# Performance work log

Measured on AMD Instinct MI355X. Metric: run time of the kernel, lower is better.

The kernel has to match this reference:

```python
import jax, jax.numpy as jnp
import numpy as np

SEQ, D, HID, C = 512, 768, 128, 5
NENT, SPAN = 128, 16


def setup_inputs() -> dict:
    key = jax.random.key(0)
    ks = jax.random.split(key, 24)
    s = 0.02

    def rn(k, shape, scale=s):
        return jax.random.normal(k, shape, dtype=jnp.float32) * scale

    inp = {
        "encoder_output": rn(ks[0], (1, SEQ, D), 1.0),
        "holder_idxs": jax.random.randint(ks[1], (NENT, SPAN), 0, SEQ, dtype=jnp.int32),
        "target_idxs": jax.random.randint(ks[2], (NENT, SPAN), 0, SEQ, dtype=jnp.int32),
        "exp_idxs": jax.random.randint(ks[3], (NENT, SPAN), 0, SEQ, dtype=jnp.int32),
    }
    names = ["Wh_f", "bh_f", "Wh_b", "bh_b", "Wt_f", "bt_f", "Wt_b", "bt_b",
             "We_f", "be_f", "We_b", "be_b"]
    for n, k in zip(names, ks[4:16]):
        shape = (4 * HID, D) if n.startswith("W") else (4 * HID,)
        inp[n] = rn(k, shape)
    inp["T_he"] = rn(ks[16], (2 * HID, 2 * HID, 2 * HID))
    inp["T_te"] = rn(ks[17], (2 * HID, 2 * HID, 2 * HID))
    inp["T_cls"] = rn(ks[18], (2 * HID, C, 2 * HID))
    return inp


def _lstm_cell_step(x, W_ih, b):
    # Single LSTM step with h0=c0=0 (the torch module feeds seq_len=1 to nn.LSTM,
    # so W_hh @ h0 vanishes; b = b_ih + b_hh). Gate order: i, f, g, o.
    g = x @ W_ih.T + b                         # [n, L, 4H]
    i, f, gg, o = jnp.split(g, 4, axis=-1)
    c = jax.nn.sigmoid(i) * jnp.tanh(gg)
    return jax.nn.sigmoid(o) * jnp.tanh(c)     # h, [n, L, H]


def _lstm_pool(enc_seq, idxs, Wf, bf, Wb, bb):
    toks = enc_seq[idxs]                       # [n, L, D] gather
    h = jnp.concatenate([_lstm_cell_step(toks, Wf, bf),
                         _lstm_cell_step(toks, Wb, bb)], axis=-1)  # [n, L, 2H]
    return h.max(axis=1)                       # max-pool over span -> [n, 2H]


def reference(encoder_output, holder_idxs, target_idxs, exp_idxs,
              Wh_f, bh_f, Wh_b, bh_b, Wt_f, bt_f, Wt_b, bt_b,
              We_f, be_f, We_b, be_b, T_he, T_te, T_cls):
    enc = encoder_output[0]                    # [SEQ, D]
    He = _lstm_pool(enc, holder_idxs, Wh_f, bh_f, Wh_b, bh_b)   # [nh, 2H]
    Te = _lstm_pool(enc, target_idxs, Wt_f, bt_f, Wt_b, bt_b)   # [nt, 2H]
    Ee = _lstm_pool(enc, exp_idxs, We_f, be_f, We_b, be_b)      # [ne, 2H]

    # hep[i,k] = He[i] @ T_he @ Ee[k];  tep[j,k] = Te[j] @ T_te @ Ee[k]
    hep = jnp.einsum('ia,abc,kc->ikb', He, T_he, Ee)            # [nh, ne, 2H]
    tep = jnp.einsum('ja,abc,kc->jkb', Te, T_te, Ee)            # [nt, ne, 2H]
    # pred[i,j,k,m] = tep[j,k] @ T_cls[:,m,:] @ hep[i,k]
    pred = jnp.einsum('jkb,bmc,ikc->ijkm', tep, T_cls, hep)     # [nh, nt, ne, C]
    return pred
```

## Files before the change

### kernel.cpp

```cpp
#include <hip/hip_runtime.h>
#include <hip/hip_bf16.h>
#include <math.h>

#define DIM   768
#define HID   128
#define H2    256
#define NENT  128
#define SPAN  16
#define NCLS  5

#define POOLB_OFF 0
#define HEPB_OFF  196608
#define TEPB_OFF  (HEPB_OFF + 8388608)
#define TCLSB_OFF (TEPB_OFF + 8388608)
#define WB_OFF    (TCLSB_OFF + 655360)
#define TOKB_OFF  21168128
#define GATES_OFF (TOKB_OFF + 9437184)
#define TMPT0_OFF 21168128
#define TMPT1_OFF (TMPT0_OFF + 16777216)
#define PREDT_OFF 21168128

typedef __attribute__((ext_vector_type(8))) short bf16x8;
typedef __attribute__((ext_vector_type(4))) float f32x4;

__device__ __forceinline__ float sigmoidf_(float x) { return 1.0f / (1.0f + __expf(-x)); }

__device__ __forceinline__ unsigned short f2bf(float x) {
    __hip_bfloat16 h = __float2bfloat16(x);
    return *reinterpret_cast<unsigned short*>(&h);
}

__global__ __launch_bounds__(256)
void prep_kernel(const float* __restrict__ Whf, const float* __restrict__ Whb,
                 const float* __restrict__ Wtf, const float* __restrict__ Wtb,
                 const float* __restrict__ Wef, const float* __restrict__ Web,
                 const float* __restrict__ Tcls, const float* __restrict__ enc,
                 const int* __restrict__ idx_h, const int* __restrict__ idx_t,
                 const int* __restrict__ idx_e,
                 unsigned short* __restrict__ WB, unsigned short* __restrict__ TB,
                 unsigned short* __restrict__ tokB)
{
    const int bb = blockIdx.x;
    const int tid = threadIdx.x;
    if (bb < 1728) {
        int gid = bb * 256 + tid;
        int t2  = gid / 73728;
        int rem = gid % 73728;
        int n   = rem / 192;
        int c4  = rem % 192;
        int gate = n >> 7, j = n & 127;
        int srow = (gate == 0) ? j : (gate == 1) ? 256 + j : 384 + j;
        const float* W = (t2 == 0) ? Whf : (t2 == 1) ? Whb : (t2 == 2) ? Wtf :
                         (t2 == 3) ? Wtb : (t2 == 4) ? Wef : Web;
        float4 v = ((const float4*)(W + srow * DIM))[c4];
        unsigned short* d = WB + ((size_t)(t2 * 384 + n)) * DIM + c4 * 4;
        d[0] = f2bf(v.x); d[1] = f2bf(v.y); d[2] = f2bf(v.z); d[3] = f2bf(v.w);
    } else if (bb < 3008) {
        int idx = (bb - 1728) * 256 + tid;
        int b = idx / (NCLS * H2);
        int r = idx % (NCLS * H2);
        int m = r >> 8, c = r & 255;
        TB[((m << 8) + c) * H2 + b] = f2bf(Tcls[idx]);
    } else {
        int gid = (bb - 3008) * 256 + tid;
        int r  = gid / 192, c4 = gid % 192;
        int type = r >> 11;
        int rem  = r & 2047;
        const int* idx = (type == 0) ? idx_h : (type == 1) ? idx_t : idx_e;
        int row = idx[rem];
        float4 v = ((const float4*)(enc + (size_t)row * DIM))[c4];
        unsigned short h4[4] = { f2bf(v.x), f2bf(v.y), f2bf(v.z), f2bf(v.w) };
        *(uint2*)(tokB + (size_t)r * DIM + c4 * 4) = *(uint2*)h4;
    }
}

__global__ __launch_bounds__(256)
void gates_mfma(const unsigned short* __restrict__ tokB,
                const unsigned short* __restrict__ WB,
                float* __restrict__ gates)
{
    __shared__ unsigned short As[2][128 * 64];
    __shared__ unsigned short Bs[2][128 * 64];
    const int lbid = ((int)blockIdx.x & 7) * 36 + ((int)blockIdx.x >> 3);
    const int type = lbid / 96;
    const int rem  = lbid % 96;
    const int mb0  = (rem / 6) * 128;
    const int nb0  = (rem % 6) * 128;
    const int tid = threadIdx.x;
    const int w = tid >> 6, l = tid & 63;
    const int lr = l & 15, lg = l >> 4;
    const unsigned short* A = tokB + (size_t)type * 2048 * DIM + (size_t)mb0 * DIM;
    const unsigned short* B = WB   + (size_t)type * 768  * DIM + (size_t)nb0 * DIM;

    const int sr0 = tid >> 3;
    const int sc  = tid & 7;

    bf16x8 ra[4], rb[4];
    #define LOADT(kt)                                                        \
        {                                                                    \
            const int koff = (kt) * 64 + sc * 8;                             \
            _Pragma("unroll")                                                \
            for (int p = 0; p < 4; ++p) {                                    \
                int rr = sr0 + p * 32;                                       \
                ra[p] = *(const bf16x8*)(A + (size_t)rr * DIM + koff);       \
                rb[p] = *(const bf16x8*)(B + (size_t)rr * DIM + koff);       \
            }                                                                \
        }
    #define WRITET(buf)                                                      \
        {                                                                    \
            _Pragma("unroll")                                                \
            for (int p = 0; p < 4; ++p) {                                    \
                int rr = sr0 + p * 32;                                       \
                int bo = (rr * 128 + sc * 16) ^ ((rr & 7) << 4);             \
                *(bf16x8*)((char*)As[buf] + bo) = ra[p];                     \
                *(bf16x8*)((char*)Bs[buf] + bo) = rb[p];                     \
            }                                                                \
        }

    f32x4 acc[4][4];
    #pragma unroll
    for (int mt = 0; mt < 4; ++mt)
        #pragma unroll
        for (int nt = 0; nt < 4; ++nt) acc[mt][nt] = (f32x4){0.f, 0.f, 0.f, 0.f};

    const int am0 = (w & 1) * 64;
    const int bn0 = (w >> 1) * 64;

    LOADT(0);
    WRITET(0);
    __syncthreads();

    int cur = 0;
    #pragma unroll 1
    for (int kt = 0; kt < 12; ++kt) {
        if (kt + 1 < 12) LOADT(kt + 1);

        #pragma unroll
        for (int ks = 0; ks < 2; ++ks) {
            bf16x8 af[4], bf[4];
            #pragma unroll
            for (int mt = 0; mt < 4; ++mt) {
                int rr = am0 + mt * 16 + lr;
                int bo = (rr * 128 + ks * 64 + lg * 16) ^ ((rr & 7) << 4);
                af[mt] = *(const bf16x8*)((const char*)As[cur] + bo);
            }
            #pragma unroll
            for (int nt = 0; nt < 4; ++nt) {
                int rr = bn0 + nt * 16 + lr;
                int bo = (rr * 128 + ks * 64 + lg * 16) ^ ((rr & 7) << 4);
                bf[nt] = *(const bf16x8*)((const char*)Bs[cur] + bo);
            }
            #pragma unroll
            for (int mt = 0; mt < 4; ++mt)
                #pragma unroll
                for (int nt = 0; nt < 4; ++nt)
                    acc[mt][nt] = __builtin_amdgcn_mfma_f32_16x16x32_bf16(af[mt], bf[nt], acc[mt][nt], 0, 0, 0);
        }

        if (kt + 1 < 12) {
            WRITET(cur ^ 1);
        }
        __syncthreads();
        cur ^= 1;
    }
    #undef LOADT
    #undef WRITET

    float* C = gates + (size_t)type * 2048 * 768 + (size_t)mb0 * 768 + nb0;
    #pragma unroll
    for (int mt = 0; mt < 4; ++mt)
        #pragma unroll
        for (int nt = 0; nt < 4; ++nt)
            #pragma unroll
            for (int r = 0; r < 4; ++r)
                C[(size_t)(am0 + mt * 16 + lg * 4 + r) * 768 + bn0 + nt * 16 + lr] = acc[mt][nt][r];
}

__global__ __launch_bounds__(256)
void pool_epilogue(const float* __restrict__ gates,
                   const float* __restrict__ bhf, const float* __restrict__ bhb,
                   const float* __restrict__ btf, const float* __restrict__ btb,
                   const float* __restrict__ bef, const float* __restrict__ beb,
                   unsigned short* __restrict__ poolB)
{
    const int type = blockIdx.x >> 7;
    const int ent  = blockIdx.x & 127;
    const int tid  = threadIdx.x;
    const int dir  = tid >> 7;
    const int j    = tid & 127;
    const float* Bv = (type == 0) ? (dir ? bhb : bhf)
                    : (type == 1) ? (dir ? btb : btf)
                                  : (dir ? beb : bef);
    const float bi = Bv[j], bg = Bv[2 * HID + j], bo = Bv[3 * HID + j];
    const float* g0 = gates + ((size_t)type * 2048 + ent * 16) * 768 + dir * 384 + j;
    float hmax = -1e30f;
    #pragma unroll
    for (int l = 0; l < SPAN; ++l) {
        const float* gr = g0 + l * 768;
        float iv = sigmoidf_(gr[0]   + bi);
        float gv = tanhf(   gr[128] + bg);
        float ov = sigmoidf_(gr[256] + bo);
        hmax = fmaxf(hmax, ov * tanhf(iv * gv));
    }
    poolB[(size_t)(type * NENT + ent) * H2 + dir * HID + j] = f2bf(hmax);
}

__global__ __launch_bounds__(512)
void gemm1_mfma(const unsigned short* __restrict__ EeB,
                const float* __restrict__ T0, const float* __restrict__ T1,
                unsigned short* __restrict__ tmpT0, unsigned short* __restrict__ tmpT1)
{
    __shared__ unsigned short Ts[2][256 * 64];
    const int bid = blockIdx.x;
    const int tz = bid >> 8;
    const int b  = bid & 255;
    const float* T = tz ? T1 : T0;
    unsigned short* outp = tz ? tmpT1 : tmpT0;
    const int tid = threadIdx.x;
    const int w = tid >> 6, l = tid & 63;
    const int lr = l & 15, lg = l >> 4;
    const int kw = (w & 1) * 64;
    const int aw = (w >> 1) * 64;

    const int sr0 = tid >> 3;
    const int sc  = tid & 7;

    float4 rv[4][2];
    #define G1LOAD(kt)                                                            \
        {                                                                         \
            _Pragma("unroll")                                                     \
            for (int p = 0; p < 4; ++p) {                                         \
                const float* tr = T + ((size_t)(sr0 + p * 64) * 256 + b) * 256    \
                                    + (kt) * 64 + sc * 8;                         \
                rv[p][0] = ((const float4*)tr)[0];                                \
                rv[p][1] = ((const float4*)tr)[1];                                \
            }                                                                     \
        }
    #define G1WRITE(buf)                                                          \
        {                                                                         \
            _Pragma("unroll")                                                     \
            for (int p = 0; p < 4; ++p) {                                         \
                int rr = sr0 + p * 64;                                            \
                bf16x8 hv; unsigned short* hp = (unsigned short*)&hv;             \
                hp[0]=f2bf(rv[p][0].x); hp[1]=f2bf(rv[p][0].y);                   \
                hp[2]=f2bf(rv[p][0].z); hp[3]=f2bf(rv[p][0].w);                   \
                hp[4]=f2bf(rv[p][1].x); hp[5]=f2bf(rv[p][1].y);                   \
                hp[6]=f2bf(rv[p][1].z); hp[7]=f2bf(rv[p][1].w);                   \
                int bo = (rr * 128 + sc * 16) ^ ((rr & 7) << 4);                  \
                *(bf16x8*)((char*)Ts[buf] + bo) = hv;                             \
            }                                                                     \
        }

    f32x4 acc[4][4];
    #pragma unroll
    for (int mt = 0; mt < 4; ++mt)
        #pragma unroll
        for (int nt = 0; nt < 4; ++nt) acc[mt][nt] = (f32x4){0.f, 0.f, 0.f, 0.f};

    G1LOAD(0);
    G1WRITE(0);
    __syncthreads();

    int cur = 0;
    #pragma unroll 1
    for (int kt = 0; kt < 4; ++kt) {
        if (kt + 1 < 4) G1LOAD(kt + 1);

        #pragma unroll
        for (int ks = 0; ks < 2; ++ks) {
            bf16x8 af[4], bf[4];
            #pragma unroll
            for (int mt = 0; mt < 4; ++mt)
                af[mt] = *(const bf16x8*)(EeB + (kw + mt * 16 + lr) * H2 + kt * 64 + ks * 32 + lg * 8);
            #pragma unroll
            for (int nt = 0; nt < 4; ++nt) {
                int rr = aw + nt * 16 + lr;
                int bo = (rr * 128 + ks * 64 + lg * 16) ^ ((rr & 7) << 4);
                bf[nt] = *(const bf16x8*)((const char*)Ts[cur] + bo);
            }
            #pragma unroll
            for (int mt = 0; mt < 4; ++mt)
                #pragma unroll
                for (int nt = 0; nt < 4; ++nt)
                    acc[mt][nt] = __builtin_amdgcn_mfma_f32_16x16x32_bf16(af[mt], bf[nt], acc[mt][nt], 0, 0, 0);
        }

        if (kt + 1 < 4) G1WRITE(cur ^ 1);
        __syncthreads();
        cur ^= 1;
    }
    #undef G1LOAD
    #undef G1WRITE

    #pragma unroll
    for (int mt = 0; mt < 4; ++mt)
        #pragma unroll
        for (int nt = 0; nt < 4; ++nt)
            #pragma unroll
            for (int r = 0; r < 4; ++r) {
                int k  = kw + mt * 16 + lg * 4 + r;
                int a_ = aw + nt * 16 + lr;
                outp[(size_t)k * 65536 + b * 256 + a_] = f2bf(acc[mt][nt][r]);
            }
}

__global__ __launch_bounds__(256)
void gemm2_mfma(const unsigned short* __restrict__ HeB, const unsigned short* __restrict__ TeB,
                const unsigned short* __restrict__ tmpT0, const unsigned short* __restrict__ tmpT1,
                unsigned short* __restrict__ hepB, unsigned short* __restrict__ tepB)
{
    const int bid = blockIdx.x;
    const int t  = bid >> 8;
    const int k  = (bid >> 1) & 127;
    const int nb0 = (bid & 1) * 128;
    const unsigned short* HxB = t ? TeB : HeB;
    const unsigned short* Bp  = (t ? tmpT1 : tmpT0) + (size_t)k * 65536;
    unsigned short* outB = t ? tepB : hepB;
    const int tid = threadIdx.x;
    const int w = tid >> 6, l = tid & 63;
    const int lr = l & 15, lg = l >> 4;
    const int bb = w * 32;

    f32x4 acc[8][2];
    #pragma unroll
    for (int mt = 0; mt < 8; ++mt)
        #pragma unroll
        for (int nt = 0; nt < 2; ++nt) acc[mt][nt] = (f32x4){0.f, 0.f, 0.f, 0.f};

    #pragma unroll 2
    for (int ks = 0; ks < 8; ++ks) {
        bf16x8 af[8], bf[2];
        #pragma unroll
        for (int mt = 0; mt < 8; ++mt)
            af[mt] = *(const bf16x8*)(HxB + (mt * 16 + lr) * H2 + ks * 32 + lg * 8);
        #pragma unroll
        for (int nt = 0; nt < 2; ++nt)
            bf[nt] = *(const bf16x8*)(Bp + (nb0 + bb + nt * 16 + lr) * H2 + ks * 32 + lg * 8);
        #pragma unroll
        for (int mt = 0; mt < 8; ++mt)
            #pragma unroll
            for (int nt = 0; nt < 2; ++nt)
                acc[mt][nt] = __builtin_amdgcn_mfma_f32_16x16x32_bf16(af[mt], bf[nt], acc[mt][nt], 0, 0, 0);
    }
    #pragma unroll
    for (int mt = 0; mt < 8; ++mt)
        #pragma unroll
        for (int nt = 0; nt < 2; ++nt)
            #pragma unroll
            for (int r = 0; r < 4; ++r) {
                int i = mt * 16 + lg * 4 + r;
                int bc = nb0 + bb + nt * 16 + lr;
                outB[(size_t)k * (NENT * H2) + i * H2 + bc] = f2bf(acc[mt][nt][r]);
            }
}

__global__ __launch_bounds__(512)
void step3_mfma(const unsigned short* __restrict__ hepB,
                const unsigned short* __restrict__ tepB,
                const unsigned short* __restrict__ TclsB,
                float* __restrict__ predT)
{
    __shared__ unsigned short tepS[64 * 256];
    __shared__ unsigned short WS[64 * 256];
    const int lbid = (blockIdx.x & 7) * 32 + (blockIdx.x >> 3);
    const int k  = lbid >> 1;
    const int jh = lbid & 1;
    const int tid = threadIdx.x;
    const int w  = tid >> 6;
    const int l  = tid & 63;
    const int lr = l & 15;
    const int lg = l >> 4;
    const int swz = (lr & 7) << 4;

    {
        const unsigned short* tk = tepB + (size_t)k * (NENT * H2) + (size_t)jh * 64 * H2;
        int row = tid >> 5;
        int col = (tid & 31) * 8;
        #pragma unroll
        for (int q = 0; q < 4; ++q) {
            int r = row + q * 16;
            bf16x8 v = *(const bf16x8*)(tk + r * H2 + col);
            int byteoff = (((r << 8) + col) << 1) ^ ((r & 7) << 4);
            *(bf16x8*)((char*)tepS + byteoff) = v;
        }
    }

    bf16x8 ha[8];
    {
        const unsigned short* hk = hepB + (size_t)k * (NENT * H2);
        #pragma unroll
        for (int ks = 0; ks < 8; ++ks)
            ha[ks] = *(const bf16x8*)(hk + (w * 16 + lr) * H2 + ks * 32 + lg * 8);
    }
    __syncthreads();

    #pragma unroll 1
    for (int m = 0; m < NCLS; ++m) {
        {
            const unsigned short* tcm = TclsB + (size_t)m * (H2 * H2);
            f32x4 acc1[4][2];
            #pragma unroll
            for (int jt = 0; jt < 4; ++jt)
                #pragma unroll
                for (int ct = 0; ct < 2; ++ct) acc1[jt][ct] = (f32x4){0.f, 0.f, 0.f, 0.f};

            #pragma unroll
            for (int ks = 0; ks < 8; ++ks) {
                bf16x8 a[4], bb[2];
                #pragma unroll
                for (int jt = 0; jt < 4; ++jt) {
                    int byteoff = ((((jt * 16 + lr) << 8) + ks * 32 + lg * 8) << 1) ^ swz;
                    a[jt] = *(const bf16x8*)((const char*)tepS + byteoff);
                }
                #pragma unroll
                for (int ct = 0; ct < 2; ++ct)
                    bb[ct] = *(const bf16x8*)(tcm + (size_t)(w * 32 + ct * 16 + lr) * H2 + ks * 32 + lg * 8);
                #pragma unroll
                for (int jt = 0; jt < 4; ++jt)
                    #pragma unroll
                    for (int ct = 0; ct < 2; ++ct)
                        acc1[jt][ct] = __builtin_amdgcn_mfma_f32_16x16x32_bf16(a[jt], bb[ct], acc1[jt][ct], 0, 0, 0);
            }
            #pragma unroll
            for (int jt = 0; jt < 4; ++jt)
                #pragma unroll
                for (int ct = 0; ct < 2; ++ct)
                    #pragma unroll
                    for (int r = 0; r < 4; ++r) {
                        int j = jt * 16 + lg * 4 + r;
                        int c = w * 32 + ct * 16 + lr;
                        int byteoff = ((((j << 8) + c)) << 1) ^ ((j & 7) << 4);
                        *(unsigned short*)((char*)WS + byteoff) = f2bf(acc1[jt][ct][r]);
                    }
        }
        __syncthreads();

        {
            f32x4 acc2[4];
            #pragma unroll
            for (int jt = 0; jt < 4; ++jt) acc2[jt] = (f32x4){0.f, 0.f, 0.f, 0.f};

            #pragma unroll
            for (int ks = 0; ks < 8; ++ks) {
                #pragma unroll
                for (int jt = 0; jt < 4; ++jt) {
                    int byteoff = ((((jt * 16 + lr) << 8) + ks * 32 + lg * 8) << 1) ^ swz;
                    bf16x8 wb = *(const bf16x8*)((const char*)WS + byteoff);
                    acc2[jt] = __builtin_amdgcn_mfma_f32_16x16x32_bf16(ha[ks], wb, acc2[jt], 0, 0, 0);
                }
            }
            float* po = predT + (size_t)(k * NCLS + m) * (NENT * NENT);
            #pragma unroll
            for (int jt = 0; jt < 4; ++jt)
                #pragma unroll
                for (int r = 0; r < 4; ++r) {
                    int i = w * 16 + lg * 4 + r;
                    int j = jh * 64 + jt * 16 + lr;
                    po[i * NENT + j] = acc2[jt][r];
                }
        }
        __syncthreads();
    }
}

__global__ __launch_bounds__(256)
void transpose_out(const float* __restrict__ predT, float* __restrict__ out)
{
    __shared__ float Ls[160][33];
    const int bid = blockIdx.x;
    const int ij0 = (bid >> 2) * 32;
    const int km0 = (bid & 3) * 160;
    const int t = threadIdx.x;

    #pragma unroll
    for (int q = 0; q < 20; ++q) {
        int r = (t >> 5) + q * 8;
        int c = t & 31;
        Ls[r][c] = predT[(size_t)(km0 + r) * 16384 + ij0 + c];
    }
    __syncthreads();
    for (int idx = t; idx < 32 * 160; idx += 256) {
        int r = idx / 160, c = idx % 160;
        out[(size_t)(ij0 + r) * 640 + km0 + c] = Ls[c][r];
    }
}

extern "C" void kernel_launch(void* const* d_in, const int* in_sizes, int n_in,
                              void* d_out, int out_size, void* d_ws, size_t ws_size,
                              hipStream_t stream)
{
    (void)in_sizes; (void)n_in; (void)out_size; (void)ws_size;
    const float* enc  = (const float*)d_in[0];
    const int*   hidx = (const int*)d_in[1];
    const int*   tidx = (const int*)d_in[2];
    const int*   eidx = (const int*)d_in[3];
    const float* Whf = (const float*)d_in[4];
    const float* bhf = (const float*)d_in[5];
    const float* Whb = (const float*)d_in[6];
    const float* bhb = (const float*)d_in[7];
    const float* Wtf = (const float*)d_in[8];
    const float* btf = (const float*)d_in[9];
    const float* Wtb = (const float*)d_in[10];
    const float* btb = (const float*)d_in[11];
    const float* Wef = (const float*)d_in[12];
    const float* bef = (const float*)d_in[13];
    const float* Web = (const float*)d_in[14];
    const float* beb = (const float*)d_in[15];
    const float* T_he  = (const float*)d_in[16];
    const float* T_te  = (const float*)d_in[17];
    const float* T_cls = (const float*)d_in[18];

    float* out = (float*)d_out;
    char*  ws  = (char*)d_ws;
    unsigned short* poolB = (unsigned short*)(ws + POOLB_OFF);
    unsigned short* hepB  = (unsigned short*)(ws + HEPB_OFF);
    unsigned short* tepB  = (unsigned short*)(ws + TEPB_OFF);
    unsigned short* TclsB = (unsigned short*)(ws + TCLSB_OFF);
    unsigned short* WB    = (unsigned short*)(ws + WB_OFF);
    unsigned short* tokB  = (unsigned short*)(ws + TOKB_OFF);
    float*          gates = (float*)(ws + GATES_OFF);
    unsigned short* tmpT0 = (unsigned short*)(ws + TMPT0_OFF);
    unsigned short* tmpT1 = (unsigned short*)(ws + TMPT1_OFF);
    float*          predT = (float*)(ws + PREDT_OFF);

    unsigned short* HeB = poolB;
    unsigned short* TeB = poolB + 1 * NENT * H2;
    unsigned short* EeB = poolB + 2 * NENT * H2;

    prep_kernel<<<7616, 256, 0, stream>>>(Whf, Whb, Wtf, Wtb, Wef, Web,
                                          T_cls, enc, hidx, tidx, eidx,
                                          WB, TclsB, tokB);

    gates_mfma<<<288, 256, 0, stream>>>(tokB, WB, gates);

    pool_epilogue<<<384, 256, 0, stream>>>(gates, bhf, bhb, btf, btb, bef, beb, poolB);

    gemm1_mfma<<<512, 512, 0, stream>>>(EeB, T_he, T_te, tmpT0, tmpT1);

    gemm2_mfma<<<512, 256, 0, stream>>>(HeB, TeB, tmpT0, tmpT1, hepB, tepB);

    step3_mfma<<<256, 512, 0, stream>>>(hepB, tepB, TclsB, predT);

    transpose_out<<<2048, 256, 0, stream>>>(predT, out);
}
```

Before: 154.6 us.

## Fuse the two bilinear GEMMs per b-slice and keep the intermediate in LDS

Merges gemm1 and gemm2 into one pair_mfma kernel. Each block converts a full 256x256 T slice to bf16 in 128KB of LDS, computes the Ee contraction there, and writes the bf16 intermediate back into LDS for the He/Te contraction. This removes the 32MB tmpT round-trip through global memory and one kernel launch. In exchange hep/tep are written in a b-major layout, so step3 now transposes both operands into LDS with scalar 2-byte shared stores. The 128KB LDS use limits occupancy to one block per CU.

After: 135.7 us. 1.14x faster.

```diff
diff --git a/kernel.cpp b/kernel.cpp
--- a/kernel.cpp
+++ b/kernel.cpp
@@ -16,8 +16,6 @@
 #define WB_OFF    (TCLSB_OFF + 655360)
 #define TOKB_OFF  21168128
 #define GATES_OFF (TOKB_OFF + 9437184)
-#define TMPT0_OFF 21168128
-#define TMPT1_OFF (TMPT0_OFF + 16777216)
 #define PREDT_OFF 21168128
 
 typedef __attribute__((ext_vector_type(8))) short bf16x8;
@@ -206,160 +204,130 @@
 }
 
 __global__ __launch_bounds__(512)
-void gemm1_mfma(const unsigned short* __restrict__ EeB,
-                const float* __restrict__ T0, const float* __restrict__ T1,
-                unsigned short* __restrict__ tmpT0, unsigned short* __restrict__ tmpT1)
-{
-    __shared__ unsigned short Ts[2][256 * 64];
+void pair_mfma(const unsigned short* __restrict__ EeB,
+               const unsigned short* __restrict__ HeB,
+               const unsigned short* __restrict__ TeB,
+               const float* __restrict__ T0, const float* __restrict__ T1,
+               unsigned short* __restrict__ hepN,
+               unsigned short* __restrict__ tepN)
+{
+    __shared__ __align__(16) char smem[131072];
     const int bid = blockIdx.x;
-    const int tz = bid >> 8;
-    const int b  = bid & 255;
-    const float* T = tz ? T1 : T0;
-    unsigned short* outp = tz ? tmpT1 : tmpT0;
+    const int t = bid >> 8;
+    const int b = bid & 255;
+    const float* T = t ? T1 : T0;
+    const unsigned short* Hx = t ? TeB : HeB;
+    unsigned short* outp = t ? tepN : hepN;
     const int tid = threadIdx.x;
     const int w = tid >> 6, l = tid & 63;
     const int lr = l & 15, lg = l >> 4;
-    const int kw = (w & 1) * 64;
-    const int aw = (w >> 1) * 64;
-
-    const int sr0 = tid >> 3;
-    const int sc  = tid & 7;
-
-    float4 rv[4][2];
-    #define G1LOAD(kt)                                                            \
-        {                                                                         \
-            _Pragma("unroll")                                                     \
-            for (int p = 0; p < 4; ++p) {                                         \
-                const float* tr = T + ((size_t)(sr0 + p * 64) * 256 + b) * 256    \
-                                    + (kt) * 64 + sc * 8;                         \
-                rv[p][0] = ((const float4*)tr)[0];                                \
-                rv[p][1] = ((const float4*)tr)[1];                                \
-            }                                                                     \
-        }
-    #define G1WRITE(buf)                                                          \
-        {                                                                         \
-            _Pragma("unroll")                                                     \
-            for (int p = 0; p < 4; ++p) {                                         \
-                int rr = sr0 + p * 64;                                            \
-                bf16x8 hv; unsigned short* hp = (unsigned short*)&hv;             \
-                hp[0]=f2bf(rv[p][0].x); hp[1]=f2bf(rv[p][0].y);                   \
-                hp[2]=f2bf(rv[p][0].z); hp[3]=f2bf(rv[p][0].w);                   \
-                hp[4]=f2bf(rv[p][1].x); hp[5]=f2bf(rv[p][1].y);                   \
-                hp[6]=f2bf(rv[p][1].z); hp[7]=f2bf(rv[p][1].w);                   \
-                int bo = (rr * 128 + sc * 16) ^ ((rr & 7) << 4);                  \
-                *(bf16x8*)((char*)Ts[buf] + bo) = hv;                             \
-            }                                                                     \
-        }
-
-    f32x4 acc[4][4];
-    #pragma unroll
-    for (int mt = 0; mt < 4; ++mt)
-        #pragma unroll
-        for (int nt = 0; nt < 4; ++nt) acc[mt][nt] = (f32x4){0.f, 0.f, 0.f, 0.f};
-
-    G1LOAD(0);
-    G1WRITE(0);
+
+    {
+        const int a    = tid >> 1;
+        const int chalf = (tid & 1) * 128;
+        const float* src = T + ((size_t)a * 256 + b) * 256 + chalf;
+        #pragma unroll 8
+        for (int f = 0; f < 32; ++f) {
+            float4 v = ((const float4*)src)[f];
+            unsigned short h4[4] = { f2bf(v.x), f2bf(v.y), f2bf(v.z), f2bf(v.w) };
+            int c = chalf + f * 4;
+            int bo = (a * 512 + c * 2) ^ ((a & 7) << 4);
+            *(uint2*)(smem + bo) = *(uint2*)h4;
+        }
+    }
     __syncthreads();
 
-    int cur = 0;
-    #pragma unroll 1
-    for (int kt = 0; kt < 4; ++kt) {
-        if (kt + 1 < 4) G1LOAD(kt + 1);
-
-        #pragma unroll
-        for (int ks = 0; ks < 2; ++ks) {
+    {
+        const int aw = (w & 3) * 64;
+        const int kw = (w >> 2) * 64;
+        f32x4 acc1[4][4];
+        #pragma unroll
+        for (int mt = 0; mt < 4; ++mt)
+            #pragma unroll
+            for (int nt = 0; nt < 4; ++nt) acc1[mt][nt] = (f32x4){0.f, 0.f, 0.f, 0.f};
+
+        #pragma unroll
+        for (int ks = 0; ks < 8; ++ks) {
             bf16x8 af[4], bf[4];
             #pragma unroll
+            for (int mt = 0; mt < 4; ++mt) {
+                int ar = aw + mt * 16 + lr;
+                int bo = (ar * 512 + (ks * 32 + lg * 8) * 2) ^ ((ar & 7) << 4);
+                af[mt] = *(const bf16x8*)(smem + bo);
+            }
+            #pragma unroll
+            for (int nt = 0; nt < 4; ++nt)
+                bf[nt] = *(const bf16x8*)(EeB + (kw + nt * 16 + lr) * H2 + ks * 32 + lg * 8);
+            #pragma unroll
             for (int mt = 0; mt < 4; ++mt)
-                af[mt] = *(const bf16x8*)(EeB + (kw + mt * 16 + lr) * H2 + kt * 64 + ks * 32 + lg * 8);
+                #pragma unroll
+                for (int nt = 0; nt < 4; ++nt)
+                    acc1[mt][nt] = __builtin_amdgcn_mfma_f32_16x16x32_bf16(af[mt], bf[nt], acc1[mt][nt], 0, 0, 0);
+        }
+        __syncthreads();
+
+        #pragma unroll
+        for (int mt = 0; mt < 4; ++mt)
             #pragma unroll
             for (int nt = 0; nt < 4; ++nt) {
-                int rr = aw + nt * 16 + lr;
-                int bo = (rr * 128 + ks * 64 + lg * 16) ^ ((rr & 7) << 4);
-                bf[nt] = *(const bf16x8*)((const char*)Ts[cur] + bo);
-            }
+                int k  = kw + nt * 16 + lr;
+                int a0 = aw + mt * 16 + lg * 4;
+                unsigned short h4[4] = { f2bf(acc1[mt][nt][0]), f2bf(acc1[mt][nt][1]),
+                                         f2bf(acc1[mt][nt][2]), f2bf(acc1[mt][nt][3]) };
+                int bo = (k * 512 + a0 * 2) ^ ((k & 7) << 4);
+                *(uint2*)(smem + bo) = *(uint2*)h4;
+            }
+    }
+    __syncthreads();
+
+    {
+        const int kw2 = (w & 1) * 64;
+        const int iw  = (w >> 1) * 32;
+        f32x4 acc2[4][2];
+        #pragma unroll
+        for (int mt = 0; mt < 4; ++mt)
+            #pragma unroll
+            for (int nt = 0; nt < 2; ++nt) acc2[mt][nt] = (f32x4){0.f, 0.f, 0.f, 0.f};
+
+        #pragma unroll
+        for (int ks = 0; ks < 8; ++ks) {
+            bf16x8 af[4], bf[2];
+            #pragma unroll
+            for (int mt = 0; mt < 4; ++mt) {
+                int kr = kw2 + mt * 16 + lr;
+                int bo = (kr * 512 + (ks * 32 + lg * 8) * 2) ^ ((kr & 7) << 4);
+                af[mt] = *(const bf16x8*)(smem + bo);
+            }
+            #pragma unroll
+            for (int nt = 0; nt < 2; ++nt)
+                bf[nt] = *(const bf16x8*)(Hx + (iw + nt * 16 + lr) * H2 + ks * 32 + lg * 8);
             #pragma unroll
             for (int mt = 0; mt < 4; ++mt)
                 #pragma unroll
-                for (int nt = 0; nt < 4; ++nt)
-                    acc[mt][nt] = __builtin_amdgcn_mfma_f32_16x16x32_bf16(af[mt], bf[nt], acc[mt][nt], 0, 0, 0);
-        }
-
-        if (kt + 1 < 4) G1WRITE(cur ^ 1);
-        __syncthreads();
-        cur ^= 1;
-    }
-    #undef G1LOAD
-    #undef G1WRITE
-
-    #pragma unroll
-    for (int mt = 0; mt < 4; ++mt)
-        #pragma unroll
-        for (int nt = 0; nt < 4; ++nt)
-            #pragma unroll
-            for (int r = 0; r < 4; ++r) {
-                int k  = kw + mt * 16 + lg * 4 + r;
-                int a_ = aw + nt * 16 + lr;
-                outp[(size_t)k * 65536 + b * 256 + a_] = f2bf(acc[mt][nt][r]);
-            }
-}
-
-__global__ __launch_bounds__(256)
-void gemm2_mfma(const unsigned short* __restrict__ HeB, const unsigned short* __restrict__ TeB,
-                const unsigned short* __restrict__ tmpT0, const unsigned short* __restrict__ tmpT1,
-                unsigned short* __restrict__ hepB, unsigned short* __restrict__ tepB)
-{
-    const int bid = blockIdx.x;
-    const int t  = bid >> 8;
-    const int k  = (bid >> 1) & 127;
-    const int nb0 = (bid & 1) * 128;
-    const unsigned short* HxB = t ? TeB : HeB;
-    const unsigned short* Bp  = (t ? tmpT1 : tmpT0) + (size_t)k * 65536;
-    unsigned short* outB = t ? tepB : hepB;
-    const int tid = threadIdx.x;
-    const int w = tid >> 6, l = tid & 63;
-    const int lr = l & 15, lg = l >> 4;
-    const int bb = w * 32;
-
-    f32x4 acc[8][2];
-    #pragma unroll
-    for (int mt = 0; mt < 8; ++mt)
-        #pragma unroll
-        for (int nt = 0; nt < 2; ++nt) acc[mt][nt] = (f32x4){0.f, 0.f, 0.f, 0.f};
-
-    #pragma unroll 2
-    for (int ks = 0; ks < 8; ++ks) {
-        bf16x8 af[8], bf[2];
-        #pragma unroll
-        for (int mt = 0; mt < 8; ++mt)
-            af[mt] = *(const bf16x8*)(HxB + (mt * 16 + lr) * H2 + ks * 32 + lg * 8);
-        #pragma unroll
-        for (int nt = 0; nt < 2; ++nt)
-            bf[nt] = *(const bf16x8*)(Bp + (nb0 + bb + nt * 16 + lr) * H2 + ks * 32 + lg * 8);
-        #pragma unroll
-        for (int mt = 0; mt < 8; ++mt)
+                for (int nt = 0; nt < 2; ++nt)
+                    acc2[mt][nt] = __builtin_amdgcn_mfma_f32_16x16x32_bf16(af[mt], bf[nt], acc2[mt][nt], 0, 0, 0);
+        }
+        unsigned short* po = outp + (size_t)b * (128 * 128);
+        #pragma unroll
+        for (int mt = 0; mt < 4; ++mt)
             #pragma unroll
             for (int nt = 0; nt < 2; ++nt)
-                acc[mt][nt] = __builtin_amdgcn_mfma_f32_16x16x32_bf16(af[mt], bf[nt], acc[mt][nt], 0, 0, 0);
-    }
-    #pragma unroll
-    for (int mt = 0; mt < 8; ++mt)
-        #pragma unroll
-        for (int nt = 0; nt < 2; ++nt)
-            #pragma unroll
-            for (int r = 0; r < 4; ++r) {
-                int i = mt * 16 + lg * 4 + r;
-                int bc = nb0 + bb + nt * 16 + lr;
-                outB[(size_t)k * (NENT * H2) + i * H2 + bc] = f2bf(acc[mt][nt][r]);
-            }
+                #pragma unroll
+                for (int r = 0; r < 4; ++r) {
+                    int k = kw2 + mt * 16 + lg * 4 + r;
+                    int i = iw + nt * 16 + lr;
+                    po[k * 128 + i] = f2bf(acc2[mt][nt][r]);
+                }
+    }
 }
 
 __global__ __launch_bounds__(512)
-void step3_mfma(const unsigned short* __restrict__ hepB,
-                const unsigned short* __restrict__ tepB,
+void step3_mfma(const unsigned short* __restrict__ hepN,
+                const unsigned short* __restrict__ tepN,
                 const unsigned short* __restrict__ TclsB,
                 float* __restrict__ predT)
 {
+    __shared__ unsigned short hepS[128 * 256];
     __shared__ unsigned short tepS[64 * 256];
     __shared__ unsigned short WS[64 * 256];
     const int lbid = (blockIdx.x & 7) * 32 + (blockIdx.x >> 3);
@@ -372,27 +340,39 @@
     const int lg = l >> 4;
     const int swz = (lr & 7) << 4;
 
-    {
-        const unsigned short* tk = tepB + (size_t)k * (NENT * H2) + (size_t)jh * 64 * H2;
-        int row = tid >> 5;
-        int col = (tid & 31) * 8;
+    #pragma unroll
+    for (int q = 0; q < 4; ++q) {
+        int bcol = q * 64 + l;
+        bf16x8 v = *(const bf16x8*)(tepN + ((size_t)bcol * 128 + k) * 128 + jh * 64 + w * 8);
+        #pragma unroll
+        for (int r = 0; r < 8; ++r) {
+            int j = w * 8 + r;
+            int bo = (j * 512 + bcol * 2) ^ (r << 4);
+            *(unsigned short*)((char*)tepS + bo) = ((unsigned short*)&v)[r];
+        }
+    }
+    #pragma unroll
+    for (int s = 0; s < 2; ++s)
         #pragma unroll
         for (int q = 0; q < 4; ++q) {
-            int r = row + q * 16;
-            bf16x8 v = *(const bf16x8*)(tk + r * H2 + col);
-            int byteoff = (((r << 8) + col) << 1) ^ ((r & 7) << 4);
-            *(bf16x8*)((char*)tepS + byteoff) = v;
-        }
-    }
+            int bcol = q * 64 + l;
+            bf16x8 v = *(const bf16x8*)(hepN + ((size_t)bcol * 128 + k) * 128 + w * 16 + s * 8);
+            #pragma unroll
+            for (int r = 0; r < 8; ++r) {
+                int i = w * 16 + s * 8 + r;
+                int bo = (i * 512 + bcol * 2) ^ (r << 4);
+                *(unsigned short*)((char*)hepS + bo) = ((unsigned short*)&v)[r];
+            }
+        }
+    __syncthreads();
 
     bf16x8 ha[8];
-    {
-        const unsigned short* hk = hepB + (size_t)k * (NENT * H2);
-        #pragma unroll
-        for (int ks = 0; ks < 8; ++ks)
-            ha[ks] = *(const bf16x8*)(hk + (w * 16 + lr) * H2 + ks * 32 + lg * 8);
-    }
-    __syncthreads();
+    #pragma unroll
+    for (int ks = 0; ks < 8; ++ks) {
+        int ir = w * 16 + lr;
+        int bo = (ir * 512 + (ks * 32 + lg * 8) * 2) ^ ((ir & 7) << 4);
+        ha[ks] = *(const bf16x8*)((const char*)hepS + bo);
+    }
 
     #pragma unroll 1
     for (int m = 0; m < NCLS; ++m) {
@@ -513,14 +493,12 @@
     float* out = (float*)d_out;
     char*  ws  = (char*)d_ws;
     unsigned short* poolB = (unsigned short*)(ws + POOLB_OFF);
-    unsigned short* hepB  = (unsigned short*)(ws + HEPB_OFF);
-    unsigned short* tepB  = (unsigned short*)(ws + TEPB_OFF);
+    unsigned short* hepN  = (unsigned short*)(ws + HEPB_OFF);
+    unsigned short* tepN  = (unsigned short*)(ws + TEPB_OFF);
     unsigned short* TclsB = (unsigned short*)(ws + TCLSB_OFF);
     unsigned short* WB    = (unsigned short*)(ws + WB_OFF);
     unsigned short* tokB  = (unsigned short*)(ws + TOKB_OFF);
     float*          gates = (float*)(ws + GATES_OFF);
-    unsigned short* tmpT0 = (unsigned short*)(ws + TMPT0_OFF);
-    unsigned short* tmpT1 = (unsigned short*)(ws + TMPT1_OFF);
     float*          predT = (float*)(ws + PREDT_OFF);
 
     unsigned short* HeB = poolB;
@@ -535,11 +513,9 @@
 
     pool_epilogue<<<384, 256, 0, stream>>>(gates, bhf, bhb, btf, btb, bef, beb, poolB);
 
-    gemm1_mfma<<<512, 512, 0, stream>>>(EeB, T_he, T_te, tmpT0, tmpT1);
-
-    gemm2_mfma<<<512, 256, 0, stream>>>(HeB, TeB, tmpT0, tmpT1, hepB, tepB);
-
-    step3_mfma<<<256, 512, 0, stream>>>(hepB, tepB, TclsB, predT);
+    pair_mfma<<<512, 512, 0, stream>>>(EeB, HeB, TeB, T_he, T_te, hepN, tepN);
+
+    step3_mfma<<<256, 512, 0, stream>>>(hepN, tepN, TclsB, predT);
 
     transpose_out<<<2048, 256, 0, stream>>>(predT, out);
 }
```
